# Kernel optimization log

Measured on AMD Instinct MI355X. Metric: run time of the kernel, lower is better.

Reference implementation:

```python
import jax, jax.numpy as jnp
import numpy as np

MAX_SHIFT = 64  # init kwarg; alpha=None -> score_max branch


def setup_inputs() -> dict:
    key = jax.random.key(0)
    k1, k2 = jax.random.split(key)
    x = jax.random.normal(k1, (64, 2, 4096), dtype=jnp.float32)
    y = jax.random.normal(k2, (64, 2, 4096), dtype=jnp.float32)
    return {"x": x, "y": y}


def reference(x, y):
    S = MAX_SHIFT
    W = 2 * S + 1  # num_windows
    # forward(): flip along channel axis
    x = jnp.flip(x, axis=1)
    B, C, D = x.shape
    # min-max normalize each (batch, channel) trace to [-1, 1]
    xmin = x.min(axis=-1, keepdims=True)
    xmax = x.max(axis=-1, keepdims=True)
    x = 2 * (x - xmin) / (xmax - xmin) - 1
    # torch.hann_window(dim) is periodic: 0.5*(1 - cos(2*pi*n/N))
    hann = 0.5 * (1.0 - jnp.cos(2.0 * jnp.pi * jnp.arange(D, dtype=x.dtype) / D))
    x = x * hann
    # pad by max_shift on both sides, then take W sliding windows of length D
    xpad = jnp.pad(x, ((0, 0), (0, 0), (S, S)))  # [B, C, D+2S]
    idx = jnp.arange(W)[:, None] + jnp.arange(D)[None, :]  # [W, D]
    xw = xpad[:, :, idx]  # [B, C, W, D] (matches torch unfold+reshape)
    xw = jnp.transpose(xw, (2, 0, 1, 3))  # [W, B, C, D]
    # mean-centered Pearson correlation per window
    xc = xw - xw.mean(axis=-1, keepdims=True)
    yc = y - y.mean(axis=-1, keepdims=True)
    corr = jnp.sum(xc * yc, axis=-1)  # [W, B, C]
    norm = jnp.sum(xc * xc, axis=-1) * jnp.sum(yc * yc, axis=-1)
    corr = corr / jnp.sqrt(norm)
    # alpha is None -> score_max: max over shifts, L2 over channels
    values = corr.max(axis=0)  # [B, C]
    scores = jnp.sqrt(jnp.sum(values ** 2, axis=-1))  # [B]
    return -scores.mean()
```

## Files before the change

### kernel.cpp

```cpp
#include <hip/hip_runtime.h>
#include <math.h>

#define DD      4096
#define SSHIFT  64
#define WW      129
#define PADN    (DD + 2 * SSHIFT)
#define NPART   4
#define BLOCKN  256

__global__ __launch_bounds__(BLOCKN) void spl_main(
        const float* __restrict__ x, const float* __restrict__ y,
        float* __restrict__ partial) {
    const int blk  = blockIdx.x;
    const int bc   = blk >> 2;
    const int part = blk & (NPART - 1);
    const int b = bc >> 1;
    const int c = bc & 1;
    const float* xp = x + (size_t)(b * 2 + (1 - c)) * DD;
    const float* yp = y + (size_t)(b * 2 + c) * DD;

    __shared__ float xhp[PADN];
    __shared__ float red[12];

    const int tid  = threadIdx.x;
    const int lane = tid & 63;
    const int wv   = tid >> 6;

    if (tid < SSHIFT) {
        xhp[tid] = 0.0f;
        xhp[SSHIFT + DD + tid] = 0.0f;
    }

    float xmn = 3.0e38f, xmx = -3.0e38f, ysum = 0.0f;
    for (int d = tid; d < DD; d += BLOCKN) {
        float xv = xp[d];
        xmn = fminf(xmn, xv);
        xmx = fmaxf(xmx, xv);
        ysum += yp[d];
    }
    #pragma unroll
    for (int off = 32; off > 0; off >>= 1) {
        xmn  = fminf(xmn, __shfl_down(xmn, off, 64));
        xmx  = fmaxf(xmx, __shfl_down(xmx, off, 64));
        ysum += __shfl_down(ysum, off, 64);
    }
    if (lane == 0) { red[wv] = xmn; red[4 + wv] = xmx; red[8 + wv] = ysum; }
    __syncthreads();
    xmn = fminf(fminf(red[0], red[1]), fminf(red[2], red[3]));
    xmx = fmaxf(fmaxf(red[4], red[5]), fmaxf(red[6], red[7]));
    const float ymean = (red[8] + red[9] + red[10] + red[11]) * (1.0f / (float)DD);
    const float inv   = 2.0f / (xmx - xmn);
    __syncthreads();

    for (int d = tid; d < DD; d += BLOCKN) {
        float h = 0.5f * (1.0f - cosf((float)d * (6.2831853071795864769f / (float)DD)));
        xhp[SSHIFT + d] = (inv * (xp[d] - xmn) - 1.0f) * h;
    }

    float ycr[64];
    float syy = 0.0f;
    #pragma unroll
    for (int i = 0; i < 64; ++i) {
        float yv = yp[64 * i + lane] - ymean;
        ycr[i] = yv;
        syy = fmaf(yv, yv, syy);
    }
    #pragma unroll
    for (int off = 32; off > 0; off >>= 1) syy += __shfl_down(syy, off, 64);
    syy = __shfl(syy, 0, 64);

    __syncthreads();

    float vmax = -3.0e38f;
    for (int w = part + NPART * wv; w < WW; w += NPART * 4) {
        float cr = 0.0f, sx = 0.0f, sxx = 0.0f;
        #pragma unroll
        for (int i = 0; i < 64; ++i) {
            float xv = xhp[64 * i + lane + w];
            cr  = fmaf(xv, ycr[i], cr);
            sx += xv;
            sxx = fmaf(xv, xv, sxx);
        }
        #pragma unroll
        for (int off = 32; off > 0; off >>= 1) {
            cr  += __shfl_down(cr, off, 64);
            sx  += __shfl_down(sx, off, 64);
            sxx += __shfl_down(sxx, off, 64);
        }
        if (lane == 0) {
            float varx = sxx - sx * sx * (1.0f / (float)DD);
            float corr = cr / sqrtf(varx * syy);
            vmax = fmaxf(vmax, corr);
        }
    }
    if (lane == 0) red[wv] = vmax;
    __syncthreads();
    if (tid == 0)
        partial[blk] = fmaxf(fmaxf(red[0], red[1]), fmaxf(red[2], red[3]));
}

__global__ void spl_final(const float* __restrict__ partial,
                          float* __restrict__ out) {
    const int b = threadIdx.x;
    float v0 = -3.0e38f, v1 = -3.0e38f;
    #pragma unroll
    for (int p = 0; p < NPART; ++p) {
        v0 = fmaxf(v0, partial[(b * 2 + 0) * NPART + p]);
        v1 = fmaxf(v1, partial[(b * 2 + 1) * NPART + p]);
    }
    float s = sqrtf(v0 * v0 + v1 * v1);
    #pragma unroll
    for (int off = 32; off > 0; off >>= 1) s += __shfl_down(s, off, 64);
    if (b == 0) out[0] = -s * (1.0f / 64.0f);
}

extern "C" void kernel_launch(void* const* d_in, const int* in_sizes, int n_in,
                              void* d_out, int out_size, void* d_ws, size_t ws_size,
                              hipStream_t stream) {
    const float* x = (const float*)d_in[0];
    const float* y = (const float*)d_in[1];
    float* out     = (float*)d_out;
    float* partial = (float*)d_ws;

    spl_main<<<dim3(128 * NPART), dim3(BLOCKN), 0, stream>>>(x, y, partial);
    spl_final<<<dim3(1), dim3(64), 0, stream>>>(partial, out);
}
```

Baseline: 76.38 us.

## Use prefix sums for window statistics and float4 shifted LDS layout

Each window's sum and sum of squares now come from block-wide totals minus small prefix/suffix sums over the pad regions, so the inner loop only accumulates the cross term. Each block stores its x trace shifted by its partition offset, which makes every window start aligned to four floats and allows float4 LDS reads with float4 y registers. It also vectorizes the global min/max and mean pass and uses the hardware cosine intrinsic. The cost is extra shared arrays, an additional reduction and scan phase, and possible float precision differences from computing the window variance by subtracting from the totals.

Result: faster. 71.50 us (-6.4%).

```diff
diff --git a/kernel.cpp b/kernel.cpp
--- a/kernel.cpp
+++ b/kernel.cpp
@@ -19,24 +19,26 @@
     const float* xp = x + (size_t)(b * 2 + (1 - c)) * DD;
     const float* yp = y + (size_t)(b * 2 + c) * DD;
 
-    __shared__ float xhp[PADN];
-    __shared__ float red[12];
+    __shared__ __align__(16) float xs[PADN];
+    __shared__ float P0s[65], P0q[65], Qs[65], Qq[65];
+    __shared__ float red[20];
+    __shared__ float wred[4];
 
     const int tid  = threadIdx.x;
     const int lane = tid & 63;
     const int wv   = tid >> 6;
 
-    if (tid < SSHIFT) {
-        xhp[tid] = 0.0f;
-        xhp[SSHIFT + DD + tid] = 0.0f;
-    }
-
+    const float4* xp4 = (const float4*)xp;
+    const float4* yp4 = (const float4*)yp;
     float xmn = 3.0e38f, xmx = -3.0e38f, ysum = 0.0f;
-    for (int d = tid; d < DD; d += BLOCKN) {
-        float xv = xp[d];
-        xmn = fminf(xmn, xv);
-        xmx = fmaxf(xmx, xv);
-        ysum += yp[d];
+    #pragma unroll
+    for (int it = 0; it < DD / 4 / BLOCKN; ++it) {
+        int d4 = tid + it * BLOCKN;
+        float4 xv = xp4[d4];
+        xmn = fminf(xmn, fminf(fminf(xv.x, xv.y), fminf(xv.z, xv.w)));
+        xmx = fmaxf(xmx, fmaxf(fmaxf(xv.x, xv.y), fmaxf(xv.z, xv.w)));
+        float4 yv = yp4[d4];
+        ysum += (yv.x + yv.y) + (yv.z + yv.w);
     }
     #pragma unroll
     for (int off = 32; off > 0; off >>= 1) {
@@ -50,53 +52,105 @@
     xmx = fmaxf(fmaxf(red[4], red[5]), fmaxf(red[6], red[7]));
     const float ymean = (red[8] + red[9] + red[10] + red[11]) * (1.0f / (float)DD);
     const float inv   = 2.0f / (xmx - xmn);
-    __syncthreads();
 
-    for (int d = tid; d < DD; d += BLOCKN) {
-        float h = 0.5f * (1.0f - cosf((float)d * (6.2831853071795864769f / (float)DD)));
-        xhp[SSHIFT + d] = (inv * (xp[d] - xmn) - 1.0f) * h;
+    float ssum = 0.0f, ssq = 0.0f;
+    for (int m = tid; m < PADN; m += BLOCKN) {
+        int d = m + part - SSHIFT;
+        float v = 0.0f;
+        if (d >= 0 && d < DD) {
+            float h = 0.5f * (1.0f - __builtin_amdgcn_cosf((float)d * (1.0f / (float)DD)));
+            v = (inv * (xp[d] - xmn) - 1.0f) * h;
+        }
+        xs[m] = v;
+        ssum += v;
+        ssq  = fmaf(v, v, ssq);
     }
+    #pragma unroll
+    for (int off = 32; off > 0; off >>= 1) {
+        ssum += __shfl_down(ssum, off, 64);
+        ssq  += __shfl_down(ssq,  off, 64);
+    }
+    if (lane == 0) { red[12 + wv] = ssum; red[16 + wv] = ssq; }
 
-    float ycr[64];
+    float4 yc4[16];
     float syy = 0.0f;
     #pragma unroll
-    for (int i = 0; i < 64; ++i) {
-        float yv = yp[64 * i + lane] - ymean;
-        ycr[i] = yv;
-        syy = fmaf(yv, yv, syy);
+    for (int i = 0; i < 16; ++i) {
+        float4 v = yp4[64 * i + lane];
+        v.x -= ymean; v.y -= ymean; v.z -= ymean; v.w -= ymean;
+        yc4[i] = v;
+        syy = fmaf(v.x, v.x, fmaf(v.y, v.y, fmaf(v.z, v.z, fmaf(v.w, v.w, syy))));
     }
     #pragma unroll
     for (int off = 32; off > 0; off >>= 1) syy += __shfl_down(syy, off, 64);
     syy = __shfl(syy, 0, 64);
 
     __syncthreads();
+    const float Stot  = (red[12] + red[13]) + (red[14] + red[15]);
+    const float Sqtot = (red[16] + red[17]) + (red[18] + red[19]);
 
+    if (wv == 0) {
+        float v = xs[SSHIFT - part + lane];
+        float s = v, sq = v * v, vsq = sq;
+        #pragma unroll
+        for (int off = 1; off < 64; off <<= 1) {
+            float t  = __shfl_up(s,  off, 64);
+            float tq = __shfl_up(sq, off, 64);
+            if (lane >= off) { s += t; sq += tq; }
+        }
+        P0s[lane + 1] = s; P0q[lane + 1] = sq;
+        if (lane == 0) { P0s[0] = 0.0f; P0q[0] = 0.0f; }
+        (void)vsq;
+    } else if (wv == 1) {
+        float v = xs[DD - part + lane];
+        float s = v, sq = v * v;
+        #pragma unroll
+        for (int off = 1; off < 64; off <<= 1) {
+            float t  = __shfl_up(s,  off, 64);
+            float tq = __shfl_up(sq, off, 64);
+            if (lane >= off) { s += t; sq += tq; }
+        }
+        float Ts = __shfl(s, 63, 64), Tq = __shfl(sq, 63, 64);
+        Qs[lane] = Ts - (s - v);
+        Qq[lane] = Tq - (sq - v * v);
+        if (lane == 63) { Qs[64] = 0.0f; Qq[64] = 0.0f; }
+    }
+    __syncthreads();
+
+    const float4* xs4 = (const float4*)xs;
+    const int w0 = part + 4 * wv;
     float vmax = -3.0e38f;
-    for (int w = part + NPART * wv; w < WW; w += NPART * 4) {
-        float cr = 0.0f, sx = 0.0f, sxx = 0.0f;
-        #pragma unroll
-        for (int i = 0; i < 64; ++i) {
-            float xv = xhp[64 * i + lane + w];
-            cr  = fmaf(xv, ycr[i], cr);
-            sx += xv;
-            sxx = fmaf(xv, xv, sxx);
-        }
-        #pragma unroll
-        for (int off = 32; off > 0; off >>= 1) {
-            cr  += __shfl_down(cr, off, 64);
-            sx  += __shfl_down(sx, off, 64);
-            sxx += __shfl_down(sxx, off, 64);
-        }
-        if (lane == 0) {
-            float varx = sxx - sx * sx * (1.0f / (float)DD);
-            float corr = cr / sqrtf(varx * syy);
-            vmax = fmaxf(vmax, corr);
+    #pragma unroll
+    for (int k = 0; k < 9; ++k) {
+        const int w = w0 + 16 * k;
+        if (w < WW) {
+            const int q = wv + 4 * k;
+            float cr = 0.0f;
+            #pragma unroll
+            for (int i = 0; i < 16; ++i) {
+                float4 xv = xs4[64 * i + lane + q];
+                cr = fmaf(xv.x, yc4[i].x,
+                     fmaf(xv.y, yc4[i].y,
+                     fmaf(xv.z, yc4[i].z,
+                     fmaf(xv.w, yc4[i].w, cr))));
+            }
+            #pragma unroll
+            for (int off = 32; off > 0; off >>= 1) cr += __shfl_down(cr, off, 64);
+            if (lane == 0) {
+                int hidx = (w > SSHIFT) ? (w - SSHIFT) : 0;
+                int tidx = (w < 64) ? w : 64;
+                float sx  = Stot  - P0s[hidx] - Qs[tidx];
+                float sxx = Sqtot - P0q[hidx] - Qq[tidx];
+                float varx = sxx - sx * sx * (1.0f / (float)DD);
+                float corr = cr / sqrtf(varx * syy);
+                vmax = fmaxf(vmax, corr);
+            }
         }
     }
-    if (lane == 0) red[wv] = vmax;
+    if (lane == 0) wred[wv] = vmax;
     __syncthreads();
     if (tid == 0)
-        partial[blk] = fmaxf(fmaxf(red[0], red[1]), fmaxf(red[2], red[3]));
+        partial[blk] = fmaxf(fmaxf(wred[0], wred[1]), fmaxf(wred[2], wred[3]));
 }
 
 __global__ void spl_final(const float* __restrict__ partial,
```
